# Performance work log

Measured on AMD Instinct MI355X. Metric: run time of the kernel, lower is better.

The kernel has to match this reference:

```python
import jax, jax.numpy as jnp
import numpy as np

N_NODES = 100000
N_EDGES = 1600000
D_IN = 64
D_OUT = 64
ROW_WINDOW = 16  # TCGNN row-window size (metadata only)


def setup_inputs() -> dict:
    key = jax.random.key(0)
    ks = jax.random.split(key, 7)
    X = jax.random.normal(ks[0], (N_NODES, D_IN), dtype=jnp.float32)
    weights = jax.random.normal(ks[1], (D_IN, D_OUT), dtype=jnp.float32)
    # CSR row pointers: sorted offsets into the edge list, endpoints pinned.
    rp = jnp.sort(jax.random.randint(ks[2], (N_NODES + 1,), 0, N_EDGES, dtype=jnp.int32))
    row_pointers = rp.at[0].set(0).at[-1].set(N_EDGES)
    column_index = jax.random.randint(ks[3], (N_EDGES,), 0, N_NODES, dtype=jnp.int32)
    # TCGNN tiling metadata (does not affect the math; kept for signature fidelity)
    blockPartition = jax.random.randint(ks[4], (N_NODES // ROW_WINDOW,), 0, 8, dtype=jnp.int32)
    edgeToColumn = jax.random.randint(ks[5], (N_EDGES,), 0, N_NODES, dtype=jnp.int32)
    edgeToRow = jax.random.randint(ks[6], (N_EDGES,), 0, N_NODES, dtype=jnp.int32)
    return {
        "X": X,
        "weights": weights,
        "row_pointers": row_pointers,
        "column_index": column_index,
        "blockPartition": blockPartition,
        "edgeToColumn": edgeToColumn,
        "edgeToRow": edgeToRow,
    }


def reference(X, weights, row_pointers, column_index, blockPartition, edgeToColumn, edgeToRow):
    # TCGNN.forward == unweighted CSR SpMM: X_prime[i] = sum_{j in N(i)} X[j]
    n_edges = column_index.shape[0]
    # Map each edge position to its CSR row id.
    row_ids = jnp.searchsorted(row_pointers, jnp.arange(n_edges, dtype=row_pointers.dtype), side="right") - 1
    gathered = X[column_index]  # [n_edges, d_in] irregular gather
    X_prime = jax.ops.segment_sum(gathered, row_ids, num_segments=X.shape[0])  # [n_nodes, d_in]
    return X_prime @ weights  # dense GEMM [n_nodes, d_out]
```

## Files before the change

kernel.cpp:

```cpp
#include <hip/hip_runtime.h>
#include <cstdint>
#include <cstddef>

#define D 64

typedef float    f32x4 __attribute__((ext_vector_type(4)));
typedef short    s16x8 __attribute__((ext_vector_type(8)));
typedef uint32_t u32x4 __attribute__((ext_vector_type(4)));

__device__ __forceinline__ uint32_t rne_bf16(float f) {
    uint32_t x = __float_as_uint(f);
    return (x + 0x7fffu + ((x >> 16) & 1u)) >> 16;
}
__device__ __forceinline__ float bf16lo(uint32_t u) { return __uint_as_float(u << 16); }
__device__ __forceinline__ float bf16hi(uint32_t u) { return __uint_as_float(u & 0xffff0000u); }

__global__ __launch_bounds__(256) void xw_gemm_kernel(
    const float* __restrict__ X, const float* __restrict__ W,
    uint32_t* __restrict__ XWh, int n_nodes)
{
    const int lane = threadIdx.x & 63;
    const int n = lane & 15;
    const int q = lane >> 4;

    s16x8 Af[4][2];
#pragma unroll
    for (int c = 0; c < 4; ++c)
#pragma unroll
        for (int kb = 0; kb < 2; ++kb) {
            s16x8 af;
#pragma unroll
            for (int j = 0; j < 8; ++j) {
                const int k = kb * 32 + q * 8 + j;
                af[j] = (short)rne_bf16(W[k * D + c * 16 + n]);
            }
            Af[c][kb] = af;
        }

    const int n_tiles = (n_nodes + 15) / 16;
    const int gwave = (int)((blockIdx.x * blockDim.x + threadIdx.x) >> 6);
    const int nwaves = (int)((gridDim.x * blockDim.x) >> 6);

    for (int t = gwave; t < n_tiles; t += nwaves) {
        const int m0 = t * 16;
        int arow = m0 + n;
        if (arow >= n_nodes) arow = n_nodes - 1;
        const float* xp = X + (size_t)arow * D;

        s16x8 Bf[2];
#pragma unroll
        for (int kb = 0; kb < 2; ++kb) {
            const f32x4 x0 = __builtin_nontemporal_load((const f32x4*)(xp + kb * 32 + q * 8));
            const f32x4 x1 = __builtin_nontemporal_load((const f32x4*)(xp + kb * 32 + q * 8 + 4));
            s16x8 b;
            b[0] = (short)rne_bf16(x0.x); b[1] = (short)rne_bf16(x0.y);
            b[2] = (short)rne_bf16(x0.z); b[3] = (short)rne_bf16(x0.w);
            b[4] = (short)rne_bf16(x1.x); b[5] = (short)rne_bf16(x1.y);
            b[6] = (short)rne_bf16(x1.z); b[7] = (short)rne_bf16(x1.w);
            Bf[kb] = b;
        }

        const bool live = (m0 + n) < n_nodes;
#pragma unroll
        for (int c = 0; c < 4; ++c) {
            f32x4 z = {0.f, 0.f, 0.f, 0.f};
            z = __builtin_amdgcn_mfma_f32_16x16x32_bf16(Af[c][0], Bf[0], z, 0, 0, 0);
            z = __builtin_amdgcn_mfma_f32_16x16x32_bf16(Af[c][1], Bf[1], z, 0, 0, 0);
            if (live) {
                uint2 o;
                o.x = rne_bf16(z[0]) | (rne_bf16(z[1]) << 16);
                o.y = rne_bf16(z[2]) | (rne_bf16(z[3]) << 16);
                *(uint2*)(XWh + (size_t)(m0 + n) * 32 + c * 8 + q * 2) = o;
            }
        }
    }
}

__global__ __launch_bounds__(256) void gather_out_kernel(
    const uint32_t* __restrict__ XWh, const int* __restrict__ rp,
    const int* __restrict__ ci, float* __restrict__ out, int n_nodes)
{
    const int lane = threadIdx.x & 63;
    const int o = lane >> 3;
    const int p = lane & 7;
    const int row = (int)((blockIdx.x * blockDim.x + threadIdx.x) >> 6);
    if (row >= n_nodes) return;

    const int e0 = rp[row];
    const int e1 = rp[row + 1];

    float a[8] = {0,0,0,0,0,0,0,0};
    float b[8] = {0,0,0,0,0,0,0,0};

    int e = e0;
    for (; e + 32 <= e1; e += 32) {
        const int i0 = ci[e      + o];
        const int i1 = ci[e +  8 + o];
        const int i2 = ci[e + 16 + o];
        const int i3 = ci[e + 24 + o];
        const u32x4 u0 = *(const u32x4*)(XWh + (size_t)i0 * 32 + p * 4);
        const u32x4 u1 = *(const u32x4*)(XWh + (size_t)i1 * 32 + p * 4);
        const u32x4 u2 = *(const u32x4*)(XWh + (size_t)i2 * 32 + p * 4);
        const u32x4 u3 = *(const u32x4*)(XWh + (size_t)i3 * 32 + p * 4);
#pragma unroll
        for (int k = 0; k < 4; ++k) {
            a[2*k] += bf16lo(u0[k]); a[2*k+1] += bf16hi(u0[k]);
            b[2*k] += bf16lo(u1[k]); b[2*k+1] += bf16hi(u1[k]);
            a[2*k] += bf16lo(u2[k]); a[2*k+1] += bf16hi(u2[k]);
            b[2*k] += bf16lo(u3[k]); b[2*k+1] += bf16hi(u3[k]);
        }
    }
    if (e + 16 <= e1) {
        const int i0 = ci[e     + o];
        const int i1 = ci[e + 8 + o];
        const u32x4 u0 = *(const u32x4*)(XWh + (size_t)i0 * 32 + p * 4);
        const u32x4 u1 = *(const u32x4*)(XWh + (size_t)i1 * 32 + p * 4);
#pragma unroll
        for (int k = 0; k < 4; ++k) {
            a[2*k] += bf16lo(u0[k]); a[2*k+1] += bf16hi(u0[k]);
            b[2*k] += bf16lo(u1[k]); b[2*k+1] += bf16hi(u1[k]);
        }
        e += 16;
    }
    if (e + 8 <= e1) {
        const int i0 = ci[e + o];
        const u32x4 u0 = *(const u32x4*)(XWh + (size_t)i0 * 32 + p * 4);
#pragma unroll
        for (int k = 0; k < 4; ++k) {
            a[2*k] += bf16lo(u0[k]); a[2*k+1] += bf16hi(u0[k]);
        }
        e += 8;
    }
    if (o < e1 - e) {
        const int i0 = ci[e + o];
        const u32x4 u0 = *(const u32x4*)(XWh + (size_t)i0 * 32 + p * 4);
#pragma unroll
        for (int k = 0; k < 4; ++k) {
            b[2*k] += bf16lo(u0[k]); b[2*k+1] += bf16hi(u0[k]);
        }
    }

#pragma unroll
    for (int j = 0; j < 8; ++j) {
        float v = a[j] + b[j];
        v += __shfl_xor(v, 8, 64);
        v += __shfl_xor(v, 16, 64);
        v += __shfl_xor(v, 32, 64);
        a[j] = v;
    }
    if (lane < 8) {
        f32x4 w0 = {a[0], a[1], a[2], a[3]};
        f32x4 w1 = {a[4], a[5], a[6], a[7]};
        *(f32x4*)(out + (size_t)row * D + p * 8)     = w0;
        *(f32x4*)(out + (size_t)row * D + p * 8 + 4) = w1;
    }
}

__global__ __launch_bounds__(256) void fused_kernel(
    const float* __restrict__ X, const float* __restrict__ W,
    const int* __restrict__ rp, const int* __restrict__ ci,
    float* __restrict__ out, int n_nodes)
{
    __shared__ float Wl[D * D];
    for (int i = threadIdx.x; i < D * D; i += 256) Wl[i] = W[i];
    __syncthreads();

    const int lane = threadIdx.x & 63;
    const int gwave = (int)((blockIdx.x * blockDim.x + threadIdx.x) >> 6);
    const int nwaves = (int)((gridDim.x * blockDim.x) >> 6);

    for (int row = gwave; row < n_nodes; row += nwaves) {
        int e0 = rp[row];
        int e1 = rp[row + 1];
        float acc = 0.f;
        for (int e = e0; e < e1; ++e) acc += X[ci[e] * D + lane];
        float sum = 0.f;
#pragma unroll
        for (int d = 0; d < D; ++d) {
            float a = __shfl(acc, d, 64);
            sum += a * Wl[d * D + lane];
        }
        out[row * D + lane] = sum;
    }
}

extern "C" void kernel_launch(void* const* d_in, const int* in_sizes, int n_in,
                              void* d_out, int out_size, void* d_ws, size_t ws_size,
                              hipStream_t stream)
{
    const float* X  = (const float*)d_in[0];
    const float* W  = (const float*)d_in[1];
    const int*   rp = (const int*)d_in[2];
    const int*   ci = (const int*)d_in[3];
    float* out = (float*)d_out;

    const int n_nodes = in_sizes[2] - 1;
    const size_t row_bytes = 32 * sizeof(uint32_t);
    const size_t need = (size_t)n_nodes * row_bytes;

    if (ws_size >= need) {
        uint32_t* XWh = (uint32_t*)d_ws;

        xw_gemm_kernel<<<1024, 256, 0, stream>>>(X, W, XWh, n_nodes);

        const int gather_blocks = (n_nodes + 3) / 4;
        gather_out_kernel<<<gather_blocks, 256, 0, stream>>>(XWh, rp, ci, out, n_nodes);
    } else {
        fused_kernel<<<2048, 256, 0, stream>>>(X, W, rp, ci, out, n_nodes);
    }
}
```

Baseline: 141.0 us.

## Process four CSR rows per wavefront in gather kernel with interleaved loads

The gather kernel now assigns four consecutive rows to each wavefront instead of one. It loops in lockstep over 8-edge chunks of all four rows, issuing up to four independent gathers per iteration. The goal is more memory-level parallelism and better handling of short rows, since average degree is about 16 and the old path spent many partial-chunk tail steps per row. In exchange each wave runs until its longest row finishes, which adds imbalance, and register pressure rises with 32 accumulators.

```diff
diff --git a/kernel.cpp b/kernel.cpp
--- a/kernel.cpp
+++ b/kernel.cpp
@@ -76,83 +76,88 @@
     }
 }
 
-__global__ __launch_bounds__(256) void gather_out_kernel(
+__global__ __launch_bounds__(256) void gather4_kernel(
     const uint32_t* __restrict__ XWh, const int* __restrict__ rp,
     const int* __restrict__ ci, float* __restrict__ out, int n_nodes)
 {
     const int lane = threadIdx.x & 63;
     const int o = lane >> 3;
     const int p = lane & 7;
-    const int row = (int)((blockIdx.x * blockDim.x + threadIdx.x) >> 6);
-    if (row >= n_nodes) return;
-
-    const int e0 = rp[row];
-    const int e1 = rp[row + 1];
-
-    float a[8] = {0,0,0,0,0,0,0,0};
-    float b[8] = {0,0,0,0,0,0,0,0};
-
-    int e = e0;
-    for (; e + 32 <= e1; e += 32) {
-        const int i0 = ci[e      + o];
-        const int i1 = ci[e +  8 + o];
-        const int i2 = ci[e + 16 + o];
-        const int i3 = ci[e + 24 + o];
-        const u32x4 u0 = *(const u32x4*)(XWh + (size_t)i0 * 32 + p * 4);
-        const u32x4 u1 = *(const u32x4*)(XWh + (size_t)i1 * 32 + p * 4);
-        const u32x4 u2 = *(const u32x4*)(XWh + (size_t)i2 * 32 + p * 4);
-        const u32x4 u3 = *(const u32x4*)(XWh + (size_t)i3 * 32 + p * 4);
-#pragma unroll
-        for (int k = 0; k < 4; ++k) {
-            a[2*k] += bf16lo(u0[k]); a[2*k+1] += bf16hi(u0[k]);
-            b[2*k] += bf16lo(u1[k]); b[2*k+1] += bf16hi(u1[k]);
-            a[2*k] += bf16lo(u2[k]); a[2*k+1] += bf16hi(u2[k]);
-            b[2*k] += bf16lo(u3[k]); b[2*k+1] += bf16hi(u3[k]);
-        }
-    }
-    if (e + 16 <= e1) {
-        const int i0 = ci[e     + o];
-        const int i1 = ci[e + 8 + o];
-        const u32x4 u0 = *(const u32x4*)(XWh + (size_t)i0 * 32 + p * 4);
-        const u32x4 u1 = *(const u32x4*)(XWh + (size_t)i1 * 32 + p * 4);
-#pragma unroll
-        for (int k = 0; k < 4; ++k) {
-            a[2*k] += bf16lo(u0[k]); a[2*k+1] += bf16hi(u0[k]);
-            b[2*k] += bf16lo(u1[k]); b[2*k+1] += bf16hi(u1[k]);
-        }
-        e += 16;
-    }
-    if (e + 8 <= e1) {
-        const int i0 = ci[e + o];
-        const u32x4 u0 = *(const u32x4*)(XWh + (size_t)i0 * 32 + p * 4);
-#pragma unroll
-        for (int k = 0; k < 4; ++k) {
-            a[2*k] += bf16lo(u0[k]); a[2*k+1] += bf16hi(u0[k]);
-        }
-        e += 8;
-    }
-    if (o < e1 - e) {
-        const int i0 = ci[e + o];
-        const u32x4 u0 = *(const u32x4*)(XWh + (size_t)i0 * 32 + p * 4);
-#pragma unroll
-        for (int k = 0; k < 4; ++k) {
-            b[2*k] += bf16lo(u0[k]); b[2*k+1] += bf16hi(u0[k]);
-        }
-    }
-
-#pragma unroll
-    for (int j = 0; j < 8; ++j) {
-        float v = a[j] + b[j];
-        v += __shfl_xor(v, 8, 64);
-        v += __shfl_xor(v, 16, 64);
-        v += __shfl_xor(v, 32, 64);
-        a[j] = v;
-    }
-    if (lane < 8) {
-        f32x4 w0 = {a[0], a[1], a[2], a[3]};
-        f32x4 w1 = {a[4], a[5], a[6], a[7]};
-        *(f32x4*)(out + (size_t)row * D + p * 8)     = w0;
-        *(f32x4*)(out + (size_t)row * D + p * 8 + 4) = w1;
+    const int gw = (int)((blockIdx.x * blockDim.x + threadIdx.x) >> 6);
+    const int base = __builtin_amdgcn_readfirstlane(gw) * 4;
+    if (base >= n_nodes) return;
+
+    int rpv[5];
+#pragma unroll
+    for (int k = 0; k < 5; ++k) {
+        int r = base + k;
+        if (r > n_nodes) r = n_nodes;
+        rpv[k] = rp[r];
+    }
+    int e[4], e1[4];
+#pragma unroll
+    for (int r = 0; r < 4; ++r) {
+        const bool ok = (base + r) < n_nodes;
+        e[r]  = ok ? rpv[r]     : 0;
+        e1[r] = ok ? rpv[r + 1] : 0;
+    }
+
+    float acc[4][8];
+#pragma unroll
+    for (int r = 0; r < 4; ++r)
+#pragma unroll
+        for (int j = 0; j < 8; ++j) acc[r][j] = 0.f;
+
+    while (true) {
+        bool any = false;
+#pragma unroll
+        for (int r = 0; r < 4; ++r) any = any | (e[r] < e1[r]);
+        if (!any) break;
+
+        int idx[4];
+        bool v[4];
+#pragma unroll
+        for (int r = 0; r < 4; ++r) {
+            v[r] = false;
+            if (e[r] < e1[r]) {
+                v[r] = o < (e1[r] - e[r]);
+                if (v[r]) idx[r] = ci[e[r] + o];
+            }
+        }
+        u32x4 u[4];
+#pragma unroll
+        for (int r = 0; r < 4; ++r)
+            if (v[r]) u[r] = *(const u32x4*)(XWh + (size_t)idx[r] * 32 + p * 4);
+#pragma unroll
+        for (int r = 0; r < 4; ++r) {
+            if (v[r]) {
+#pragma unroll
+                for (int k = 0; k < 4; ++k) {
+                    acc[r][2 * k]     += bf16lo(u[r][k]);
+                    acc[r][2 * k + 1] += bf16hi(u[r][k]);
+                }
+            }
+            e[r] += 8;
+        }
+    }
+
+#pragma unroll
+    for (int r = 0; r < 4; ++r) {
+#pragma unroll
+        for (int j = 0; j < 8; ++j) {
+            float vv = acc[r][j];
+            vv += __shfl_xor(vv, 8, 64);
+            vv += __shfl_xor(vv, 16, 64);
+            vv += __shfl_xor(vv, 32, 64);
+            acc[r][j] = vv;
+        }
+        const int row = base + r;
+        if (lane < 8 && row < n_nodes) {
+            f32x4 w0 = {acc[r][0], acc[r][1], acc[r][2], acc[r][3]};
+            f32x4 w1 = {acc[r][4], acc[r][5], acc[r][6], acc[r][7]};
+            *(f32x4*)(out + (size_t)row * D + p * 8)     = w0;
+            *(f32x4*)(out + (size_t)row * D + p * 8 + 4) = w1;
+        }
     }
 }
 
@@ -203,8 +208,9 @@
 
         xw_gemm_kernel<<<1024, 256, 0, stream>>>(X, W, XWh, n_nodes);
 
-        const int gather_blocks = (n_nodes + 3) / 4;
-        gather_out_kernel<<<gather_blocks, 256, 0, stream>>>(XWh, rp, ci, out, n_nodes);
+        const int nwaves = (n_nodes + 3) / 4;
+        const int gather_blocks = (nwaves + 3) / 4;
+        gather4_kernel<<<gather_blocks, 256, 0, stream>>>(XWh, rp, ci, out, n_nodes);
     } else {
         fused_kernel<<<2048, 256, 0, stream>>>(X, W, rp, ci, out, n_nodes);
     }
```

After: 145.9 us. 1.04x slower.
